# Performance work log

Measured on AMD Instinct MI355X. Metric: run time of the kernel, lower is better.

Reference implementation:

```python
import jax, jax.numpy as jnp
import numpy as np

B, C, H, W = 4, 512, 64, 64  # batch, channels (query_dim=model_dim), spatial

def _conv1x1(x, Wm, bias):
    # 1x1 conv == channel-mixing matmul: (b,c,h,w),(o,c) -> (b,o,h,w)
    return jnp.einsum('bchw,oc->bohw', x, Wm) + bias[None, :, None, None]

def setup_inputs() -> dict:
    key = jax.random.key(0)
    ks = jax.random.split(key, 9)
    s = 0.02
    return {
        'q':  jax.random.normal(ks[0], (B, C, H, W), dtype=jnp.float32),
        'Wq': jax.random.normal(ks[1], (C, C), dtype=jnp.float32) * s,
        'bq': jax.random.normal(ks[2], (C,), dtype=jnp.float32) * s,
        'Wk': jax.random.normal(ks[3], (C, C), dtype=jnp.float32) * s,
        'bk': jax.random.normal(ks[4], (C,), dtype=jnp.float32) * s,
        'Wv': jax.random.normal(ks[5], (C, C), dtype=jnp.float32) * s,
        'bv': jax.random.normal(ks[6], (C,), dtype=jnp.float32) * s,
        'Wo': jax.random.normal(ks[7], (C, C), dtype=jnp.float32) * s,
        'bo': jax.random.normal(ks[8], (C,), dtype=jnp.float32) * s,
    }

def reference(q, Wq, bq, Wk, bk, Wv, bv, Wo, bo):
    b, c, h, w = q.shape
    # separate=True, k=v=q (get_qkv defaults)
    qp = _conv1x1(q, Wq, bq)
    kp = _conv1x1(q, Wk, bk)
    vp = _conv1x1(q, Wv, bv)
    # view_in: b c h w -> b (h w) c  (single head; heads are NOT split)
    def flat(x):
        return x.reshape(b, c, h * w).transpose(0, 2, 1)  # (b, s, c)
    qf, kf, vf = flat(qp), flat(kp), flat(vp)
    scale = jnp.asarray(c, qf.dtype) ** -0.5  # q.shape[-1]^-0.5 = model_dim^-0.5
    sim = jnp.einsum('bqc,bkc->bqk', qf, kf) * scale  # (b, s, s)
    attn = jax.nn.softmax(sim, axis=-1)
    x = jnp.einsum('bqk,bkc->bqc', attn, vf)  # (b, s, c)
    x = x.transpose(0, 2, 1).reshape(b, c, h, w)  # view_out
    return _conv1x1(x, Wo, bo)
```

## Files before the change

kernel.cpp:

```cpp
#include <hip/hip_runtime.h>

typedef short bf16x8 __attribute__((ext_vector_type(8)));
typedef float f32x4 __attribute__((ext_vector_type(4)));

#define MFMA16(a, b, c) __builtin_amdgcn_mfma_f32_16x16x32_bf16((a), (b), (c), 0, 0, 0)

#define SEQ 4096
#define CD 512

#define LGKM0 asm volatile("s_waitcnt lgkmcnt(0)" ::: "memory")
#define VM0   asm volatile("s_waitcnt vmcnt(0)" ::: "memory")
#define VMC12 asm volatile("s_waitcnt vmcnt(12)" ::: "memory")

__device__ __forceinline__ unsigned short f2bf(float f) {
  unsigned u = __builtin_bit_cast(unsigned, f);
  u = u + 0x7FFFu + ((u >> 16) & 1u);
  return (unsigned short)(u >> 16);
}

__device__ __forceinline__ void gload_lds16(const void* g, void* l) {
  __builtin_amdgcn_global_load_lds(
      (const __attribute__((address_space(1))) void*)g,
      (__attribute__((address_space(3))) void*)l, 16, 0, 0);
}

__global__ __launch_bounds__(256) void convert_w(
    const float* __restrict__ Wq, const float* __restrict__ Wk,
    const float* __restrict__ Wv, const float* __restrict__ Wo,
    const float* __restrict__ bq, const float* __restrict__ bk,
    const float* __restrict__ bv, const float* __restrict__ bo,
    unsigned short* __restrict__ W4, float* __restrict__ b4) {
  int i = blockIdx.x * 256 + threadIdx.x;
  int p = i >> 18, idx = i & 262143;
  const float sc = 1.4426950408889634f * 0.04419417382415922f;
  const float* W = (p == 0) ? Wq : (p == 1) ? Wk : (p == 2) ? Wv : Wo;
  float v = W[idx] * ((p == 0) ? sc : 1.0f);
  W4[i] = f2bf(v);
  if (idx < 512) {
    const float* bb = (p == 0) ? bq : (p == 1) ? bk : (p == 2) ? bv : bo;
    b4[(p << 9) + idx] = bb[idx] * ((p == 0) ? sc : 1.0f);
  }
}

__global__ __launch_bounds__(256) void transpose_q(
    const float* __restrict__ q, unsigned short* __restrict__ qT) {
  __shared__ float tile[32][33];
  const int b = blockIdx.z, c0 = blockIdx.y * 32, s0 = blockIdx.x * 32;
  const int tx = threadIdx.x & 31, ty = threadIdx.x >> 5;
  #pragma unroll
  for (int i = 0; i < 4; i++) {
    int c = ty + i * 8;
    tile[c][tx] = q[((size_t)b * CD + c0 + c) * SEQ + s0 + tx];
  }
  __syncthreads();
  #pragma unroll
  for (int i = 0; i < 4; i++) {
    int s = ty + i * 8;
    qT[((size_t)b * SEQ + s0 + s) * CD + c0 + tx] = f2bf(tile[tx][s]);
  }
}

__device__ __forceinline__ void gemm_core2(
    const unsigned short* __restrict__ Ap, size_t lda,
    const unsigned short* __restrict__ Bp, size_t ldb, int kmax,
    unsigned short* As, unsigned short* Bs, f32x4 acc[4][4]) {
  const int t = threadIdx.x;
  const int wid = t >> 6, lane = t & 63;
  const int l15 = lane & 15, l4 = lane >> 4;
  const int wr = wid >> 1, wc = wid & 1;
  for (int k0 = 0; k0 < kmax; k0 += 64) {
    #pragma unroll
    for (int j = 0; j < 4; j++) {
      int slot = j * 256 + t;
      int row = slot >> 3, kc = slot & 7;
      int kcs = kc ^ (row & 7);
      gload_lds16(Ap + (size_t)row * lda + k0 + kcs * 8, As + (j * 256 + wid * 64) * 8);
      gload_lds16(Bp + (size_t)row * ldb + k0 + kcs * 8, Bs + (j * 256 + wid * 64) * 8);
    }
    __syncthreads();
    #pragma unroll
    for (int ks = 0; ks < 2; ks++) {
      bf16x8 af[4], bf[4];
      #pragma unroll
      for (int i = 0; i < 4; i++) {
        int ra = wr * 64 + i * 16 + l15;
        af[i] = *(const bf16x8*)(As + ra * 64 + (((ks << 2) | l4) ^ (ra & 7)) * 8);
        int rb = wc * 64 + i * 16 + l15;
        bf[i] = *(const bf16x8*)(Bs + rb * 64 + (((ks << 2) | l4) ^ (rb & 7)) * 8);
      }
      #pragma unroll
      for (int i = 0; i < 4; i++)
        #pragma unroll
        for (int j = 0; j < 4; j++)
          acc[i][j] = MFMA16(af[i], bf[j], acc[i][j]);
    }
    __syncthreads();
  }
}

__device__ __forceinline__ void gemm_core(
    const unsigned short* __restrict__ Ap, const unsigned short* __restrict__ Bp,
    unsigned short* As, unsigned short* Bs, f32x4 acc[4][4]) {
  gemm_core2(Ap, 512, Bp, 512, 512, As, Bs, acc);
}

__global__ __launch_bounds__(512, 2) void gemm_proj256(
    const unsigned short* __restrict__ qT, const unsigned short* __restrict__ W4,
    const float* __restrict__ b4,
    unsigned short* __restrict__ Qf, unsigned short* __restrict__ Kf,
    unsigned short* __restrict__ VfT) {
  __shared__ unsigned short As[2][2][128 * 64];
  __shared__ unsigned short Bs[2][2][128 * 64];

  const int tid = threadIdx.x;
  const int wid = tid >> 6, lane = tid & 63;
  const int l15 = lane & 15, l4 = lane >> 4;
  const int wm = wid >> 2, wn = wid & 3;

  const int id = blockIdx.x;
  const int xcd = id & 7;
  const int w = id >> 3;
  const int p = w >> 4;
  const int sub = w & 15;
  const int mt = (xcd << 3) | (sub >> 1);
  const int nt = sub & 1;
  const int m0 = mt * 256;
  const int n0 = nt * 256;

  const unsigned short* Ap = qT + (size_t)m0 * 512;
  const unsigned short* Bp = W4 + ((size_t)p * 512 + n0) * 512;

#define PJ_HALF(DST, SRC, HALF, K0)                                           \
  _Pragma("unroll")                                                           \
  for (int i_ = 0; i_ < 2; i_++) {                                            \
    int sg = i_ * 512 + tid;                                                  \
    int row = sg >> 3, kc = sg & 7;                                           \
    int kcs = kc ^ (row & 7);                                                 \
    gload_lds16(SRC + (size_t)((HALF) * 128 + row) * 512 + (K0) + kcs * 8,    \
                &DST[sg * 8]);                                                \
  }

  f32x4 acc[8][4];
  #pragma unroll
  for (int i = 0; i < 8; i++)
    #pragma unroll
    for (int j = 0; j < 4; j++) acc[i][j] = (f32x4){0.f, 0.f, 0.f, 0.f};

  PJ_HALF(As[0][0], Ap, 0, 0)
  PJ_HALF(As[0][1], Ap, 1, 0)
  PJ_HALF(Bs[0][0], Bp, 0, 0)
  PJ_HALF(Bs[0][1], Bp, 1, 0)
  VM0;
  __builtin_amdgcn_s_barrier();

  bf16x8 afr[4][2], bfr0[2][2], bfr1[2][2];
  const int bh = wn >> 1;
  const int brow = (wn & 1) * 64;

  for (int t = 0; t < 8; t++) {
    const int d = t & 1;
    const unsigned short* Ah = As[d][wm];
    const unsigned short* Bh = Bs[d][bh];
    const int k0n = (t + 1) * 64;
    const bool more = (t < 7);

    #pragma unroll
    for (int i = 0; i < 4; i++) {
      int r = i * 16 + l15;
      afr[i][0] = *(const bf16x8*)(Ah + r * 64 + ((l4) ^ (r & 7)) * 8);
      afr[i][1] = *(const bf16x8*)(Ah + r * 64 + ((4 | l4) ^ (r & 7)) * 8);
    }
    #pragma unroll
    for (int j = 0; j < 2; j++) {
      int r = brow + j * 16 + l15;
      bfr0[j][0] = *(const bf16x8*)(Bh + r * 64 + ((l4) ^ (r & 7)) * 8);
      bfr0[j][1] = *(const bf16x8*)(Bh + r * 64 + ((4 | l4) ^ (r & 7)) * 8);
    }
    if (more) {
      PJ_HALF(As[d ^ 1][0], Ap, 0, k0n)
      PJ_HALF(As[d ^ 1][1], Ap, 1, k0n)
    }
    __builtin_amdgcn_s_barrier();
    LGKM0;
    __builtin_amdgcn_s_setprio(1);
    #pragma unroll
    for (int ks = 0; ks < 2; ks++)
      #pragma unroll
      for (int i = 0; i < 4; i++)
        #pragma unroll
        for (int j = 0; j < 2; j++)
          acc[i][j] = MFMA16(afr[i][ks], bfr0[j][ks], acc[i][j]);
    __builtin_amdgcn_s_setprio(0);
    __builtin_amdgcn_s_barrier();

    #pragma unroll
    for (int j = 0; j < 2; j++) {
      int r = brow + (j + 2) * 16 + l15;
      bfr1[j][0] = *(const bf16x8*)(Bh + r * 64 + ((l4) ^ (r & 7)) * 8);
      bfr1[j][1] = *(const bf16x8*)(Bh + r * 64 + ((4 | l4) ^ (r & 7)) * 8);
    }
    if (more) {
      PJ_HALF(Bs[d ^ 1][0], Bp, 0, k0n)
      PJ_HALF(Bs[d ^ 1][1], Bp, 1, k0n)
    }
    __builtin_amdgcn_s_barrier();
    LGKM0;
    __builtin_amdgcn_s_setprio(1);
    #pragma unroll
    for (int ks = 0; ks < 2; ks++)
      #pragma unroll
      for (int i = 0; i < 4; i++)
        #pragma unroll
        for (int j = 0; j < 2; j++)
          acc[i][j + 2] = MFMA16(afr[i][ks], bfr1[j][ks], acc[i][j + 2]);
    __builtin_amdgcn_s_setprio(0);
    __builtin_amdgcn_s_barrier();

    #pragma unroll
    for (int i = 0; i < 4; i++) {
      int r = 64 + i * 16 + l15;
      afr[i][0] = *(const bf16x8*)(Ah + r * 64 + ((l4) ^ (r & 7)) * 8);
      afr[i][1] = *(const bf16x8*)(Ah + r * 64 + ((4 | l4) ^ (r & 7)) * 8);
    }
    __builtin_amdgcn_s_barrier();
    LGKM0;
    __builtin_amdgcn_s_setprio(1);
    #pragma unroll
    for (int ks = 0; ks < 2; ks++)
      #pragma unroll
      for (int i = 0; i < 4; i++)
        #pragma unroll
        for (int j = 0; j < 2; j++)
          acc[i + 4][j + 2] = MFMA16(afr[i][ks], bfr1[j][ks], acc[i + 4][j + 2]);
    __builtin_amdgcn_s_setprio(0);
    __builtin_amdgcn_s_barrier();

    __builtin_amdgcn_s_barrier();
    __builtin_amdgcn_s_setprio(1);
    #pragma unroll
    for (int ks = 0; ks < 2; ks++)
      #pragma unroll
      for (int i = 0; i < 4; i++)
        #pragma unroll
        for (int j = 0; j < 2; j++)
          acc[i + 4][j] = MFMA16(afr[i][ks], bfr0[j][ks], acc[i + 4][j]);
    __builtin_amdgcn_s_setprio(0);
    VM0;
    __builtin_amdgcn_s_barrier();
  }
#undef PJ_HALF

  if (p < 2) {
    unsigned short* out = (p == 0) ? Qf : Kf;
    #pragma unroll
    for (int i = 0; i < 8; i++) {
      int m = m0 + wm * 128 + i * 16 + l4 * 4;
      #pragma unroll
      for (int j = 0; j < 4; j++) {
        int n = n0 + wn * 64 + j * 16 + l15;
        float bias = b4[p * 512 + n];
        #pragma unroll
        for (int r = 0; r < 4; r++)
          out[(size_t)(m + r) * 512 + n] = f2bf(acc[i][j][r] + bias);
      }
    }
  } else {
    #pragma unroll
    for (int i = 0; i < 8; i++) {
      int m = m0 + wm * 128 + i * 16 + l4 * 4;
      int bb = m >> 12, sb = m & 4095;
      #pragma unroll
      for (int j = 0; j < 4; j++) {
        int n = n0 + wn * 64 + j * 16 + l15;
        float bias = b4[2 * 512 + n];
        ushort4 v;
        v.x = f2bf(acc[i][j][0] + bias);
        v.y = f2bf(acc[i][j][1] + bias);
        v.z = f2bf(acc[i][j][2] + bias);
        v.w = f2bf(acc[i][j][3] + bias);
        *(ushort4*)&VfT[((size_t)bb * CD + n) * SEQ + sb] = v;
      }
    }
  }
}

__global__ __launch_bounds__(512, 2) void gemm_qk256(
    const unsigned short* __restrict__ Qf, const unsigned short* __restrict__ Kf,
    unsigned short* __restrict__ P, float* __restrict__ partials,
    int bbase, int nbat) {
  __shared__ unsigned short As[2][2][128 * 64];
  __shared__ unsigned short Bs[2][2][128 * 64];
  __shared__ float ssum[2][4][4][16];

  const int tid = threadIdx.x;
  const int wid = tid >> 6, lane = tid & 63;
  const int l15 = lane & 15, l4 = lane >> 4;
  const int wm = wid >> 2, wn = wid & 3;

  const int id = blockIdx.x;
  const int xcd = id & 7;
  int z, qt, kt;
  if (nbat == 2) {
    z = xcd >> 2;
    int w = id >> 3;
    qt = ((xcd & 3) << 2) | (w >> 4);
    kt = w & 15;
  } else {
    z = 0;
    int w = id >> 3;
    qt = (xcd << 1) | (w >> 4);
    kt = w & 15;
  }
  const int b = bbase + z;
  const int m0 = kt * 256;
  const int n0 = qt * 256;

  const unsigned short* Ap = Kf + ((size_t)b * SEQ + m0) * CD;
  const unsigned short* Bp = Qf + ((size_t)b * SEQ + n0) * CD;

#define QK_HALF(DST, SRC, HALF, K0)                                           \
  _Pragma("unroll")                                                           \
  for (int i_ = 0; i_ < 2; i_++) {                                            \
    int sg = i_ * 512 + tid;                                                  \
    int row = sg >> 3, kc = sg & 7;                                           \
    int kcs = kc ^ (row & 7);                                                 \
    gload_lds16(SRC + (size_t)((HALF) * 128 + row) * CD + (K0) + kcs * 8,     \
                &DST[sg * 8]);                                                \
  }

  f32x4 acc[8][4];
  #pragma unroll
  for (int i = 0; i < 8; i++)
    #pragma unroll
    for (int j = 0; j < 4; j++) acc[i][j] = (f32x4){0.f, 0.f, 0.f, 0.f};

  QK_HALF(As[0][0], Ap, 0, 0)
  QK_HALF(As[0][1], Ap, 1, 0)
  QK_HALF(Bs[0][0], Bp, 0, 0)
  QK_HALF(Bs[0][1], Bp, 1, 0)
  VM0;
  __builtin_amdgcn_s_barrier();

  bf16x8 afr[4][2], bfr0[2][2], bfr1[2][2];
  const int bh = wn >> 1;
  const int brow = (wn & 1) * 64;

  for (int t = 0; t < 8; t++) {
    const int d = t & 1;
    const unsigned short* Ah = As[d][wm];
    const unsigned short* Bh = Bs[d][bh];
    const int k0n = (t + 1) * 64;
    const bool more = (t < 7);

    #pragma unroll
    for (int i = 0; i < 4; i++) {
      int r = i * 16 + l15;
      afr[i][0] = *(const bf16x8*)(Ah + r * 64 + ((l4) ^ (r & 7)) * 8);
      afr[i][1] = *(const bf16x8*)(Ah + r * 64 + ((4 | l4) ^ (r & 7)) * 8);
    }
    #pragma unroll
    for (int j = 0; j < 2; j++) {
      int r = brow + j * 16 + l15;
      bfr0[j][0] = *(const bf16x8*)(Bh + r * 64 + ((l4) ^ (r & 7)) * 8);
      bfr0[j][1] = *(const bf16x8*)(Bh + r * 64 + ((4 | l4) ^ (r & 7)) * 8);
    }
    if (more) {
      QK_HALF(As[d ^ 1][0], Ap, 0, k0n)
      QK_HALF(As[d ^ 1][1], Ap, 1, k0n)
    }
    __builtin_amdgcn_s_barrier();
    LGKM0;
    __builtin_amdgcn_s_setprio(1);
    #pragma unroll
    for (int ks = 0; ks < 2; ks++)
      #pragma unroll
      for (int i = 0; i < 4; i++)
        #pragma unroll
        for (int j = 0; j < 2; j++)
          acc[i][j] = MFMA16(afr[i][ks], bfr0[j][ks], acc[i][j]);
    __builtin_amdgcn_s_setprio(0);
    __builtin_amdgcn_s_barrier();

    #pragma unroll
    for (int j = 0; j < 2; j++) {
      int r = brow + (j + 2) * 16 + l15;
      bfr1[j][0] = *(const bf16x8*)(Bh + r * 64 + ((l4) ^ (r & 7)) * 8);
      bfr1[j][1] = *(const bf16x8*)(Bh + r * 64 + ((4 | l4) ^ (r & 7)) * 8);
    }
    if (more) {
      QK_HALF(Bs[d ^ 1][0], Bp, 0, k0n)
      QK_HALF(Bs[d ^ 1][1], Bp, 1, k0n)
    }
    __builtin_amdgcn_s_barrier();
    LGKM0;
    __builtin_amdgcn_s_setprio(1);
    #pragma unroll
    for (int ks = 0; ks < 2; ks++)
      #pragma unroll
      for (int i = 0; i < 4; i++)
        #pragma unroll
        for (int j = 0; j < 2; j++)
          acc[i][j + 2] = MFMA16(afr[i][ks], bfr1[j][ks], acc[i][j + 2]);
    __builtin_amdgcn_s_setprio(0);
    __builtin_amdgcn_s_barrier();

    #pragma unroll
    for (int i = 0; i < 4; i++) {
      int r = 64 + i * 16 + l15;
      afr[i][0] = *(const bf16x8*)(Ah + r * 64 + ((l4) ^ (r & 7)) * 8);
      afr[i][1] = *(const bf16x8*)(Ah + r * 64 + ((4 | l4) ^ (r & 7)) * 8);
    }
    __builtin_amdgcn_s_barrier();
    LGKM0;
    __builtin_amdgcn_s_setprio(1);
    #pragma unroll
    for (int ks = 0; ks < 2; ks++)
      #pragma unroll
      for (int i = 0; i < 4; i++)
        #pragma unroll
        for (int j = 0; j < 2; j++)
          acc[i + 4][j + 2] = MFMA16(afr[i][ks], bfr1[j][ks], acc[i + 4][j + 2]);
    __builtin_amdgcn_s_setprio(0);
    __builtin_amdgcn_s_barrier();

    __builtin_amdgcn_s_barrier();
    __builtin_amdgcn_s_setprio(1);
    #pragma unroll
    for (int ks = 0; ks < 2; ks++)
      #pragma unroll
      for (int i = 0; i < 4; i++)
        #pragma unroll
        for (int j = 0; j < 2; j++)
          acc[i + 4][j] = MFMA16(afr[i][ks], bfr0[j][ks], acc[i + 4][j]);
    __builtin_amdgcn_s_setprio(0);
    VM0;
    __builtin_amdgcn_s_barrier();
  }
#undef QK_HALF

  unsigned short* Pz = P + (size_t)z * SEQ * SEQ;
  float sj[4] = {0.f, 0.f, 0.f, 0.f};
  #pragma unroll
  for (int i = 0; i < 8; i++) {
    int m = m0 + wm * 128 + i * 16 + l4 * 4;
    #pragma unroll
    for (int j = 0; j < 4; j++) {
      int n = n0 + wn * 64 + j * 16 + l15;
      float p0 = __builtin_amdgcn_exp2f(acc[i][j][0]);
      float p1 = __builtin_amdgcn_exp2f(acc[i][j][1]);
      float p2 = __builtin_amdgcn_exp2f(acc[i][j][2]);
      float p3 = __builtin_amdgcn_exp2f(acc[i][j][3]);
      sj[j] += (p0 + p1) + (p2 + p3);
      ushort4 pk;
      pk.x = f2bf(p0); pk.y = f2bf(p1); pk.z = f2bf(p2); pk.w = f2bf(p3);
      *(ushort4*)&Pz[(size_t)n * SEQ + m] = pk;
    }
  }
  #pragma unroll
  for (int j = 0; j < 4; j++) {
    float s = sj[j];
    s += __shfl_xor(s, 16, 64);
    s += __shfl_xor(s, 32, 64);
    if (lane < 16) ssum[wm][wn][j][l15] = s;
  }
  __syncthreads();
  if (tid < 256) {
    int wn_ = tid >> 6, j_ = (tid >> 4) & 3, l_ = tid & 15;
    float s = ssum[0][wn_][j_][l_] + ssum[1][wn_][j_][l_];
    partials[((size_t)z * SEQ + n0 + tid) * 16 + kt] = s;
  }
}

__global__ __launch_bounds__(256) void reduce_l(
    const float* __restrict__ partials, float* __restrict__ linv) {
  int i = blockIdx.x * 256 + threadIdx.x;
  const float* p = partials + (size_t)i * 16;
  float s = 0.f;
  #pragma unroll
  for (int j = 0; j < 16; j++) s += p[j];
  linv[i] = 1.0f / s;
}

__global__ __launch_bounds__(256) void gemm_pv(
    const unsigned short* __restrict__ VfT, const unsigned short* __restrict__ P,
    const float* __restrict__ linv, unsigned short* __restrict__ Ao, int bbase) {
  __shared__ unsigned short As[128 * 64], Bs[64 * 64];
  const int z = blockIdx.z, b = bbase + z;
  const int n0 = blockIdx.x * 64, m0 = blockIdx.y * 128;
  const int t = threadIdx.x;
  const int wid = t >> 6, lane = t & 63;
  const int l15 = lane & 15, l4 = lane >> 4;
  const int wr = wid >> 1, wc = wid & 1;
  const unsigned short* Ap = VfT + ((size_t)b * CD + m0) * SEQ;
  const unsigned short* Bp = P + (size_t)z * SEQ * SEQ + (size_t)n0 * SEQ;

  f32x4 acc[4][2];
  #pragma unroll
  for (int i = 0; i < 4; i++) {
    acc[i][0] = (f32x4){0.f, 0.f, 0.f, 0.f};
    acc[i][1] = (f32x4){0.f, 0.f, 0.f, 0.f};
  }

  for (int k0 = 0; k0 < SEQ; k0 += 64) {
    #pragma unroll
    for (int j = 0; j < 4; j++) {
      int slot = j * 256 + t;
      int row = slot >> 3, kc = slot & 7;
      int kcs = kc ^ (row & 7);
      gload_lds16(Ap + (size_t)row * SEQ + k0 + kcs * 8, As + (j * 256 + wid * 64) * 8);
    }
    #pragma unroll
    for (int j = 0; j < 2; j++) {
      int slot = j * 256 + t;
      int row = slot >> 3, kc = slot & 7;
      int kcs = kc ^ (row & 7);
      gload_lds16(Bp + (size_t)row * SEQ + k0 + kcs * 8, Bs + (j * 256 + wid * 64) * 8);
    }
    __syncthreads();
    #pragma unroll
    for (int ks = 0; ks < 2; ks++) {
      bf16x8 af[4], bf[2];
      #pragma unroll
      for (int i = 0; i < 4; i++) {
        int ra = wr * 64 + i * 16 + l15;
        af[i] = *(const bf16x8*)(As + ra * 64 + (((ks << 2) | l4) ^ (ra & 7)) * 8);
      }
      #pragma unroll
      for (int j = 0; j < 2; j++) {
        int rb = wc * 32 + j * 16 + l15;
        bf[j] = *(const bf16x8*)(Bs + rb * 64 + (((ks << 2) | l4) ^ (rb & 7)) * 8);
      }
      #pragma unroll
      for (int i = 0; i < 4; i++)
        #pragma unroll
        for (int j = 0; j < 2; j++)
          acc[i][j] = MFMA16(af[i], bf[j], acc[i][j]);
    }
    __syncthreads();
  }

  #pragma unroll
  for (int j = 0; j < 2; j++) {
    int n = n0 + wc * 32 + j * 16 + l15;
    float inv = linv[(size_t)z * SEQ + n];
    #pragma unroll
    for (int i = 0; i < 4; i++) {
      int m = m0 + wr * 64 + i * 16 + l4 * 4;
      ushort4 o4;
      o4.x = f2bf(acc[i][j][0] * inv);
      o4.y = f2bf(acc[i][j][1] * inv);
      o4.z = f2bf(acc[i][j][2] * inv);
      o4.w = f2bf(acc[i][j][3] * inv);
      *(ushort4*)&Ao[((size_t)b * SEQ + n) * CD + m] = o4;
    }
  }
}

#define SECTION(T, VRC, VRP, DOPV)                                              \
  {                                                                             \
    const int t_ = (T);                                                         \
    const unsigned short* vt_ = vbase + t_ * 32;                                \
    _Pragma("unroll")                                                           \
    for (int i = 0; i < 8; i++)                                                 \
      VRC[i] = *(const bf16x8*)(vt_ + (size_t)i * 16 * SEQ);                    \
    f32x4 sf = (f32x4){0.f, 0.f, 0.f, 0.f};                                     \
    __builtin_amdgcn_s_setprio(1);                                              \
    {                                                                           \
      const char* krow = (const char*)(Ks + (size_t)(t_ & 3) * 16384) +         \
                         (s * 16 + l15) * 1024;                                 \
      const int kswz = (l15 & 7) << 4;                                          \
      _Pragma("unroll")                                                         \
      for (int ck = 0; ck < 16; ck++) {                                         \
        bf16x8 kf = *(const bf16x8*)(krow + ((ck * 64 + l4 * 16) ^ kswz));      \
        sf = MFMA16(kf, qreg[ck], sf);                                          \
      }                                                                         \
    }                                                                           \
    if (DOPV) {                                                                 \
      _Pragma("unroll")                                                         \
      for (int jf = 0; jf < 2; jf++) {                                          \
        int qv = qw * 32 + jf * 16 + l15;                                       \
        bf16x8 pb = *(const bf16x8*)((const char*)Ps + ((t_ + 1) & 1) * 4096 +  \
                                     qv * 64 +                                  \
                                     ((l4 * 16) ^ (((qv >> 1) & 3) << 4)));     \
        _Pragma("unroll")                                                       \
        for (int i = 0; i < 8; i++)                                             \
          acc[i][jf] = MFMA16(VRP[i], pb, acc[i][jf]);                          \
      }                                                                         \
    }                                                                           \
    __builtin_amdgcn_s_setprio(0);                                              \
    {                                                                           \
      float p0 = __builtin_amdgcn_exp2f(sf[0]);                                 \
      float p1 = __builtin_amdgcn_exp2f(sf[1]);                                 \
      float p2 = __builtin_amdgcn_exp2f(sf[2]);                                 \
      float p3 = __builtin_amdgcn_exp2f(sf[3]);                                 \
      l_acc[0] += p0; l_acc[1] += p1; l_acc[2] += p2; l_acc[3] += p3;           \
      ushort4 pk;                                                               \
      pk.x = f2bf(p0); pk.y = f2bf(p1); pk.z = f2bf(p2); pk.w = f2bf(p3);       \
      int q_ = g * 16 + l15;                                                    \
      int off = (t_ & 1) * 4096 + q_ * 64 +                                     \
                ((s * 32 + l4 * 8) ^ (((q_ >> 1) & 3) << 4));                   \
      *(ushort4*)((char*)Ps + off) = pk;                                        \
    }                                                                           \
    {                                                                           \
      int tt = (t_ + 2 < 128) ? t_ + 2 : 127;                                   \
      const unsigned short* kn = kbT + (size_t)tt * 32 * CD;                    \
      unsigned short* kdst = Ks + (size_t)((t_ + 2) & 3) * 16384;               \
      _Pragma("unroll")                                                         \
      for (int i = 0; i < 4; i++) {                                             \
        int slot = i * 512 + tid;                                               \
        int row = slot >> 6, kc = slot & 63;                                    \
        int kcs = kc ^ (row & 7);                                               \
        gload_lds16(kn + (size_t)row * CD + kcs * 8,                            \
                    kdst + (size_t)(i * 512 + wid * 64) * 8);                   \
      }                                                                         \
    }                                                                           \
    LGKM0;                                                                      \
    VMC12;                                                                      \
    __builtin_amdgcn_s_barrier();                                               \
  }

__global__ __launch_bounds__(512, 2) void flash_attn(
    const unsigned short* __restrict__ Qf, const unsigned short* __restrict__ Kf,
    const unsigned short* __restrict__ VfT, unsigned short* __restrict__ Ao) {
  __shared__ unsigned short Ks[4 * 32 * 512];
  __shared__ unsigned short Ps[2 * 64 * 32];
  __shared__ float ssum[4][2][16];

  const int tid = threadIdx.x;
  const int wid = tid >> 6, lane = tid & 63;
  const int l15 = lane & 15, l4 = lane >> 4;
  const int s = wid & 1, g = wid >> 1;
  const int cw = wid & 3, qw = wid >> 2;

  const int id = blockIdx.x;
  const int xcd = id & 7;
  const int b = xcd >> 1;
  const int q0 = ((id >> 3) + ((xcd & 1) << 5)) * 64;

  const unsigned short* kbT = Kf + (size_t)b * SEQ * CD;
  const unsigned short* vbase = VfT + ((size_t)b * CD + cw * 128 + l15) * SEQ + l4 * 8;

  #pragma unroll
  for (int tt = 0; tt < 2; tt++) {
    const unsigned short* kn = kbT + (size_t)tt * 32 * CD;
    unsigned short* kdst = Ks + (size_t)tt * 16384;
    #pragma unroll
    for (int i = 0; i < 4; i++) {
      int slot = i * 512 + tid;
      int row = slot >> 6, kc = slot & 63;
      int kcs = kc ^ (row & 7);
      gload_lds16(kn + (size_t)row * CD + kcs * 8, kdst + (size_t)(i * 512 + wid * 64) * 8);
    }
  }

  bf16x8 qreg[16];
  {
    const unsigned short* qp = Qf + ((size_t)b * SEQ + q0 + g * 16 + l15) * CD + l4 * 8;
    #pragma unroll
    for (int ck = 0; ck < 16; ck++) qreg[ck] = *(const bf16x8*)(qp + ck * 32);
  }

  f32x4 acc[8][2];
  #pragma unroll
  for (int i = 0; i < 8; i++) {
    acc[i][0] = (f32x4){0.f, 0.f, 0.f, 0.f};
    acc[i][1] = (f32x4){0.f, 0.f, 0.f, 0.f};
  }
  f32x4 l_acc = (f32x4){0.f, 0.f, 0.f, 0.f};

  bf16x8 vrA[8], vrB[8];

  VM0;
  __builtin_amdgcn_s_barrier();

  SECTION(0, vrA, vrB, 0);
  for (int t = 1; t < 127; t += 2) {
    SECTION(t, vrB, vrA, 1);
    SECTION(t + 1, vrA, vrB, 1);
  }
  SECTION(127, vrB, vrA, 1);

  #pragma unroll
  for (int jf = 0; jf < 2; jf++) {
    int qv = qw * 32 + jf * 16 + l15;
    bf16x8 pb = *(const bf16x8*)((const char*)Ps + 4096 + qv * 64 +
                                 ((l4 * 16) ^ (((qv >> 1) & 3) << 4)));
    #pragma unroll
    for (int i = 0; i < 8; i++)
      acc[i][jf] = MFMA16(vrB[i], pb, acc[i][jf]);
  }

  float strip = (l_acc[0] + l_acc[1]) + (l_acc[2] + l_acc[3]);
  strip += __shfl_xor(strip, 16, 64);
  strip += __shfl_xor(strip, 32, 64);
  __syncthreads();
  if (lane < 16) ssum[g][s][l15] = strip;
  __syncthreads();

  #pragma unroll
  for (int jf = 0; jf < 2; jf++) {
    int gq = qw * 2 + jf;
    float inv = 1.0f / (ssum[gq][0][l15] + ssum[gq][1][l15]);
    #pragma unroll
    for (int i = 0; i < 8; i++) {
      int c0 = cw * 128 + i * 16 + l4 * 4;
      ushort4 o4;
      o4.x = f2bf(acc[i][jf][0] * inv);
      o4.y = f2bf(acc[i][jf][1] * inv);
      o4.z = f2bf(acc[i][jf][2] * inv);
      o4.w = f2bf(acc[i][jf][3] * inv);
      *(ushort4*)&Ao[((size_t)b * SEQ + q0 + qw * 32 + jf * 16 + l15) * CD + c0] = o4;
    }
  }
}

__global__ __launch_bounds__(256) void gemm_out(
    const unsigned short* __restrict__ W4, const float* __restrict__ b4,
    const unsigned short* __restrict__ Ao, float* __restrict__ out) {
  __shared__ unsigned short As[128 * 64], Bs[128 * 64];
  const int b = blockIdx.z;
  const int n0 = blockIdx.x * 128, m0 = blockIdx.y * 128;
  f32x4 acc[4][4];
  #pragma unroll
  for (int i = 0; i < 4; i++)
    #pragma unroll
    for (int j = 0; j < 4; j++) acc[i][j] = (f32x4){0.f, 0.f, 0.f, 0.f};
  gemm_core(W4 + ((size_t)3 * 512 + m0) * 512, Ao + ((size_t)b * SEQ + n0) * 512, As, Bs, acc);

  const int t = threadIdx.x;
  const int wid = t >> 6, lane = t & 63;
  const int l15 = lane & 15, l4 = lane >> 4;
  const int wr = wid >> 1, wc = wid & 1;
  #pragma unroll
  for (int i = 0; i < 4; i++) {
    int m = m0 + wr * 64 + i * 16 + l4 * 4;
    #pragma unroll
    for (int j = 0; j < 4; j++) {
      int n = n0 + wc * 64 + j * 16 + l15;
      #pragma unroll
      for (int r = 0; r < 4; r++)
        out[((size_t)b * CD + m + r) * SEQ + n] = acc[i][j][r] + b4[3 * 512 + m + r];
    }
  }
}

extern "C" void kernel_launch(void* const* d_in, const int* in_sizes, int n_in,
                              void* d_out, int out_size, void* d_ws, size_t ws_size,
                              hipStream_t stream) {
  (void)in_sizes; (void)n_in; (void)out_size;
  const float* q  = (const float*)d_in[0];
  const float* Wq = (const float*)d_in[1];
  const float* bq = (const float*)d_in[2];
  const float* Wk = (const float*)d_in[3];
  const float* bk = (const float*)d_in[4];
  const float* Wv = (const float*)d_in[5];
  const float* bv = (const float*)d_in[6];
  const float* Wo = (const float*)d_in[7];
  const float* bo = (const float*)d_in[8];
  float* out = (float*)d_out;

  char* ws = (char*)d_ws;
  const size_t MB = (size_t)1 << 20;
  unsigned short* qT  = (unsigned short*)(ws);
  unsigned short* Qf  = (unsigned short*)(ws + 16 * MB);
  unsigned short* Kf  = (unsigned short*)(ws + 32 * MB);
  unsigned short* VfT = (unsigned short*)(ws + 48 * MB);
  unsigned short* W4  = (unsigned short*)(ws + 64 * MB);
  float* b4           = (float*)(ws + 66 * MB);
  unsigned short* Pbuf = (unsigned short*)(ws + 67 * MB);
  unsigned short* Ao = qT;

  convert_w<<<4096, 256, 0, stream>>>(Wq, Wk, Wv, Wo, bq, bk, bv, bo, W4, b4);
  transpose_q<<<dim3(128, 16, 4), 256, 0, stream>>>(q, qT);
  gemm_proj256<<<384, 512, 0, stream>>>(qT, W4, b4, Qf, Kf, VfT);

  if (ws_size >= 134 * MB) {
    float* partials = (float*)(ws + 131 * MB);
    float* linv     = (float*)(ws + (132 * MB + 512 * 1024));
    for (int pr = 0; pr < 2; ++pr) {
      gemm_qk256<<<512, 512, 0, stream>>>(Qf, Kf, Pbuf, partials, pr * 2, 2);
      reduce_l<<<32, 256, 0, stream>>>(partials, linv);
      gemm_pv<<<dim3(64, 4, 2), 256, 0, stream>>>(VfT, Pbuf, linv, Ao, pr * 2);
    }
  } else if (ws_size >= 101 * MB) {
    float* partials = (float*)(ws + 99 * MB);
    float* linv     = (float*)(ws + (99 * MB + 768 * 1024));
    for (int bb = 0; bb < 4; ++bb) {
      gemm_qk256<<<256, 512, 0, stream>>>(Qf, Kf, Pbuf, partials, bb, 1);
      reduce_l<<<16, 256, 0, stream>>>(partials, linv);
      gemm_pv<<<dim3(64, 4, 1), 256, 0, stream>>>(VfT, Pbuf, linv, Ao, bb);
    }
  } else {
    flash_attn<<<256, 512, 0, stream>>>(Qf, Kf, VfT, Ao);
  }

  gemm_out<<<dim3(32, 4, 4), 256, 0, stream>>>(W4, b4, Ao, out);
}
```

Before: 281.5 us.

## Store attention probabilities and V in fp8 and use fp8 MFMA for PV

The unnormalized softmax probabilities P are now written as fp8 (e4m3) instead of bf16. The projection kernel also emits an fp8 copy of V. The PV GEMM is rewritten to use 16x16x32 fp8 MFMA with 128-wide K tiles, and all four batches are processed in one launch with XCD-aware block mapping. This halves the traffic on the large P buffer and uses the higher fp8 MFMA throughput, at the cost of reduced precision in P and V. The workspace layout is reshuffled so that P8 reuses the old VfT region.

```diff
diff --git a/kernel.cpp b/kernel.cpp
--- a/kernel.cpp
+++ b/kernel.cpp
@@ -2,8 +2,10 @@
 
 typedef short bf16x8 __attribute__((ext_vector_type(8)));
 typedef float f32x4 __attribute__((ext_vector_type(4)));
+typedef long i64frag;
 
 #define MFMA16(a, b, c) __builtin_amdgcn_mfma_f32_16x16x32_bf16((a), (b), (c), 0, 0, 0)
+#define MFMA8(a, b, c) __builtin_amdgcn_mfma_f32_16x16x32_fp8_fp8((a), (b), (c), 0, 0, 0)
 
 #define SEQ 4096
 #define CD 512
@@ -16,6 +18,12 @@
   unsigned u = __builtin_bit_cast(unsigned, f);
   u = u + 0x7FFFu + ((u >> 16) & 1u);
   return (unsigned short)(u >> 16);
+}
+
+__device__ __forceinline__ int pk4_fp8(float p0, float p1, float p2, float p3) {
+  int w = __builtin_amdgcn_cvt_pk_fp8_f32(p0, p1, 0, false);
+  w = __builtin_amdgcn_cvt_pk_fp8_f32(p2, p3, w, true);
+  return w;
 }
 
 __device__ __forceinline__ void gload_lds16(const void* g, void* l) {
@@ -108,7 +116,7 @@
     const unsigned short* __restrict__ qT, const unsigned short* __restrict__ W4,
     const float* __restrict__ b4,
     unsigned short* __restrict__ Qf, unsigned short* __restrict__ Kf,
-    unsigned short* __restrict__ VfT) {
+    unsigned short* __restrict__ VfT, unsigned char* __restrict__ Vf8) {
   __shared__ unsigned short As[2][2][128 * 64];
   __shared__ unsigned short Bs[2][2][128 * 64];
 
@@ -273,12 +281,13 @@
       for (int j = 0; j < 4; j++) {
         int n = n0 + wn * 64 + j * 16 + l15;
         float bias = b4[2 * 512 + n];
+        float v0 = acc[i][j][0] + bias, v1 = acc[i][j][1] + bias;
+        float v2 = acc[i][j][2] + bias, v3 = acc[i][j][3] + bias;
         ushort4 v;
-        v.x = f2bf(acc[i][j][0] + bias);
-        v.y = f2bf(acc[i][j][1] + bias);
-        v.z = f2bf(acc[i][j][2] + bias);
-        v.w = f2bf(acc[i][j][3] + bias);
+        v.x = f2bf(v0); v.y = f2bf(v1); v.z = f2bf(v2); v.w = f2bf(v3);
         *(ushort4*)&VfT[((size_t)bb * CD + n) * SEQ + sb] = v;
+        if (Vf8)
+          *(int*)&Vf8[((size_t)bb * CD + n) * SEQ + sb] = pk4_fp8(v0, v1, v2, v3);
       }
     }
   }
@@ -286,7 +295,7 @@
 
 __global__ __launch_bounds__(512, 2) void gemm_qk256(
     const unsigned short* __restrict__ Qf, const unsigned short* __restrict__ Kf,
-    unsigned short* __restrict__ P, float* __restrict__ partials,
+    unsigned char* __restrict__ P8, float* __restrict__ partials,
     int bbase, int nbat) {
   __shared__ unsigned short As[2][2][128 * 64];
   __shared__ unsigned short Bs[2][2][128 * 64];
@@ -300,10 +309,10 @@
   const int id = blockIdx.x;
   const int xcd = id & 7;
   int z, qt, kt;
-  if (nbat == 2) {
-    z = xcd >> 2;
+  if (nbat == 4) {
+    z = xcd >> 1;
     int w = id >> 3;
-    qt = ((xcd & 3) << 2) | (w >> 4);
+    qt = ((xcd & 1) << 3) | (w >> 4);
     kt = w & 15;
   } else {
     z = 0;
@@ -438,7 +447,7 @@
   }
 #undef QK_HALF
 
-  unsigned short* Pz = P + (size_t)z * SEQ * SEQ;
+  unsigned char* Pz = P8 + (size_t)z * SEQ * SEQ;
   float sj[4] = {0.f, 0.f, 0.f, 0.f};
   #pragma unroll
   for (int i = 0; i < 8; i++) {
@@ -451,9 +460,7 @@
       float p2 = __builtin_amdgcn_exp2f(acc[i][j][2]);
       float p3 = __builtin_amdgcn_exp2f(acc[i][j][3]);
       sj[j] += (p0 + p1) + (p2 + p3);
-      ushort4 pk;
-      pk.x = f2bf(p0); pk.y = f2bf(p1); pk.z = f2bf(p2); pk.w = f2bf(p3);
-      *(ushort4*)&Pz[(size_t)n * SEQ + m] = pk;
+      *(int*)&Pz[(size_t)n * SEQ + m] = pk4_fp8(p0, p1, p2, p3);
     }
   }
   #pragma unroll
@@ -481,18 +488,36 @@
   linv[i] = 1.0f / s;
 }
 
-__global__ __launch_bounds__(256) void gemm_pv(
-    const unsigned short* __restrict__ VfT, const unsigned short* __restrict__ P,
-    const float* __restrict__ linv, unsigned short* __restrict__ Ao, int bbase) {
-  __shared__ unsigned short As[128 * 64], Bs[64 * 64];
-  const int z = blockIdx.z, b = bbase + z;
-  const int n0 = blockIdx.x * 64, m0 = blockIdx.y * 128;
-  const int t = threadIdx.x;
-  const int wid = t >> 6, lane = t & 63;
+__global__ __launch_bounds__(256) void gemm_pv8(
+    const unsigned char* __restrict__ Vf8, const unsigned char* __restrict__ P8,
+    const float* __restrict__ linv, unsigned short* __restrict__ Ao,
+    int bbase, int nbat) {
+  __shared__ unsigned char As[128 * 128];
+  __shared__ unsigned char Bs[64 * 128];
+  const int tid = threadIdx.x;
+  const int wid = tid >> 6, lane = tid & 63;
   const int l15 = lane & 15, l4 = lane >> 4;
   const int wr = wid >> 1, wc = wid & 1;
-  const unsigned short* Ap = VfT + ((size_t)b * CD + m0) * SEQ;
-  const unsigned short* Bp = P + (size_t)z * SEQ * SEQ + (size_t)n0 * SEQ;
+
+  const int id = blockIdx.x;
+  const int xcd = id & 7;
+  int z, qt, ct;
+  if (nbat == 4) {
+    z = xcd >> 1;
+    int w = id >> 3;
+    qt = ((xcd & 1) << 5) | (w >> 2);
+    ct = w & 3;
+  } else {
+    z = 0;
+    int w = id >> 3;
+    qt = (xcd << 3) | (w >> 2);
+    ct = w & 3;
+  }
+  const int b = bbase + z;
+  const int n0 = qt * 64, m0 = ct * 128;
+
+  const unsigned char* Ap = Vf8 + ((size_t)b * CD + m0) * SEQ;
+  const unsigned char* Bp = P8 + (size_t)z * SEQ * SEQ + (size_t)n0 * SEQ;
 
   f32x4 acc[4][2];
   #pragma unroll
@@ -501,40 +526,42 @@
     acc[i][1] = (f32x4){0.f, 0.f, 0.f, 0.f};
   }
 
-  for (int k0 = 0; k0 < SEQ; k0 += 64) {
-    #pragma unroll
-    for (int j = 0; j < 4; j++) {
-      int slot = j * 256 + t;
-      int row = slot >> 3, kc = slot & 7;
+  for (int k0 = 0; k0 < SEQ; k0 += 128) {
+    #pragma unroll
+    for (int i = 0; i < 4; i++) {
+      int sg = i * 256 + tid;
+      int row = sg >> 3, kc = sg & 7;
       int kcs = kc ^ (row & 7);
-      gload_lds16(Ap + (size_t)row * SEQ + k0 + kcs * 8, As + (j * 256 + wid * 64) * 8);
-    }
-    #pragma unroll
-    for (int j = 0; j < 2; j++) {
-      int slot = j * 256 + t;
-      int row = slot >> 3, kc = slot & 7;
+      gload_lds16(Ap + (size_t)row * SEQ + k0 + kcs * 16, As + sg * 16);
+    }
+    #pragma unroll
+    for (int i = 0; i < 2; i++) {
+      int sg = i * 256 + tid;
+      int row = sg >> 3, kc = sg & 7;
       int kcs = kc ^ (row & 7);
-      gload_lds16(Bp + (size_t)row * SEQ + k0 + kcs * 8, Bs + (j * 256 + wid * 64) * 8);
+      gload_lds16(Bp + (size_t)row * SEQ + k0 + kcs * 16, Bs + sg * 16);
     }
     __syncthreads();
     #pragma unroll
-    for (int ks = 0; ks < 2; ks++) {
-      bf16x8 af[4], bf[2];
+    for (int ks = 0; ks < 4; ks++) {
+      i64frag af[4], bf[2];
+      const int ch = ks * 2 + (l4 >> 1);
+      const int hb = (l4 & 1) * 8;
       #pragma unroll
       for (int i = 0; i < 4; i++) {
         int ra = wr * 64 + i * 16 + l15;
-        af[i] = *(const bf16x8*)(As + ra * 64 + (((ks << 2) | l4) ^ (ra & 7)) * 8);
+        af[i] = *(const i64frag*)(As + ra * 128 + (ch ^ (ra & 7)) * 16 + hb);
       }
       #pragma unroll
       for (int j = 0; j < 2; j++) {
         int rb = wc * 32 + j * 16 + l15;
-        bf[j] = *(const bf16x8*)(Bs + rb * 64 + (((ks << 2) | l4) ^ (rb & 7)) * 8);
+        bf[j] = *(const i64frag*)(Bs + rb * 128 + (ch ^ (rb & 7)) * 16 + hb);
       }
       #pragma unroll
       for (int i = 0; i < 4; i++)
         #pragma unroll
         for (int j = 0; j < 2; j++)
-          acc[i][j] = MFMA16(af[i], bf[j], acc[i][j]);
+          acc[i][j] = MFMA8(af[i], bf[j], acc[i][j]);
     }
     __syncthreads();
   }
@@ -765,34 +792,47 @@
   unsigned short* Qf  = (unsigned short*)(ws + 16 * MB);
   unsigned short* Kf  = (unsigned short*)(ws + 32 * MB);
   unsigned short* VfT = (unsigned short*)(ws + 48 * MB);
-  unsigned short* W4  = (unsigned short*)(ws + 64 * MB);
-  float* b4           = (float*)(ws + 66 * MB);
-  unsigned short* Pbuf = (unsigned short*)(ws + 67 * MB);
   unsigned short* Ao = qT;
 
-  convert_w<<<4096, 256, 0, stream>>>(Wq, Wk, Wv, Wo, bq, bk, bv, bo, W4, b4);
-  transpose_q<<<dim3(128, 16, 4), 256, 0, stream>>>(q, qT);
-  gemm_proj256<<<384, 512, 0, stream>>>(qT, W4, b4, Qf, Kf, VfT);
-
   if (ws_size >= 134 * MB) {
-    float* partials = (float*)(ws + 131 * MB);
-    float* linv     = (float*)(ws + (132 * MB + 512 * 1024));
-    for (int pr = 0; pr < 2; ++pr) {
-      gemm_qk256<<<512, 512, 0, stream>>>(Qf, Kf, Pbuf, partials, pr * 2, 2);
-      reduce_l<<<32, 256, 0, stream>>>(partials, linv);
-      gemm_pv<<<dim3(64, 4, 2), 256, 0, stream>>>(VfT, Pbuf, linv, Ao, pr * 2);
-    }
+    unsigned char* P8    = (unsigned char*)(ws + 48 * MB);
+    unsigned short* W4   = (unsigned short*)(ws + 112 * MB);
+    float* b4            = (float*)(ws + 114 * MB);
+    unsigned char* Vf8   = (unsigned char*)(ws + 115 * MB);
+    float* partials      = (float*)(ws + 123 * MB);
+    float* linv          = (float*)(ws + 124 * MB + 512 * 1024);
+
+    convert_w<<<4096, 256, 0, stream>>>(Wq, Wk, Wv, Wo, bq, bk, bv, bo, W4, b4);
+    transpose_q<<<dim3(128, 16, 4), 256, 0, stream>>>(q, qT);
+    gemm_proj256<<<384, 512, 0, stream>>>(qT, W4, b4, Qf, Kf, VfT, Vf8);
+    gemm_qk256<<<1024, 512, 0, stream>>>(Qf, Kf, P8, partials, 0, 4);
+    reduce_l<<<64, 256, 0, stream>>>(partials, linv);
+    gemm_pv8<<<1024, 256, 0, stream>>>(Vf8, P8, linv, Ao, 0, 4);
+    gemm_out<<<dim3(32, 4, 4), 256, 0, stream>>>(W4, b4, Ao, out);
   } else if (ws_size >= 101 * MB) {
-    float* partials = (float*)(ws + 99 * MB);
-    float* linv     = (float*)(ws + (99 * MB + 768 * 1024));
+    unsigned char* P8    = (unsigned char*)(ws + 48 * MB);
+    unsigned short* W4   = (unsigned short*)(ws + 64 * MB);
+    float* b4            = (float*)(ws + 66 * MB);
+    unsigned char* Vf8   = (unsigned char*)(ws + 67 * MB);
+    float* partials      = (float*)(ws + 75 * MB);
+    float* linv          = (float*)(ws + 76 * MB);
+
+    convert_w<<<4096, 256, 0, stream>>>(Wq, Wk, Wv, Wo, bq, bk, bv, bo, W4, b4);
+    transpose_q<<<dim3(128, 16, 4), 256, 0, stream>>>(q, qT);
+    gemm_proj256<<<384, 512, 0, stream>>>(qT, W4, b4, Qf, Kf, VfT, Vf8);
     for (int bb = 0; bb < 4; ++bb) {
-      gemm_qk256<<<256, 512, 0, stream>>>(Qf, Kf, Pbuf, partials, bb, 1);
+      gemm_qk256<<<256, 512, 0, stream>>>(Qf, Kf, P8, partials, bb, 1);
       reduce_l<<<16, 256, 0, stream>>>(partials, linv);
-      gemm_pv<<<dim3(64, 4, 1), 256, 0, stream>>>(VfT, Pbuf, linv, Ao, bb);
-    }
+      gemm_pv8<<<256, 256, 0, stream>>>(Vf8, P8, linv, Ao, bb, 1);
+    }
+    gemm_out<<<dim3(32, 4, 4), 256, 0, stream>>>(W4, b4, Ao, out);
   } else {
+    unsigned short* W4 = (unsigned short*)(ws + 64 * MB);
+    float* b4          = (float*)(ws + 66 * MB);
+    convert_w<<<4096, 256, 0, stream>>>(Wq, Wk, Wv, Wo, bq, bk, bv, bo, W4, b4);
+    transpose_q<<<dim3(128, 16, 4), 256, 0, stream>>>(q, qT);
+    gemm_proj256<<<384, 512, 0, stream>>>(qT, W4, b4, Qf, Kf, VfT, (unsigned char*)nullptr);
     flash_attn<<<256, 512, 0, stream>>>(Qf, Kf, VfT, Ao);
-  }
-
-  gemm_out<<<dim3(32, 4, 4), 256, 0, stream>>>(W4, b4, Ao, out);
-}
+    gemm_out<<<dim3(32, 4, 4), 256, 0, stream>>>(W4, b4, Ao, out);
+  }
+}
```

Measured after the change: 238.2 us. 15.4% less time.
